# Performance work log

Hardware: AMD Instinct MI355X
Metric: run time of the kernel (lower is better)

Reference implementation:

```python
import jax, jax.numpy as jnp
import numpy as np

DIM, N_HEAD, N_KV, HEAD_DIM = 2048, 16, 4, 128
ROPE_BASE = 10000.0
ROPE_FACTOR = 1.0  # YaRN with factor=1 == plain RoPE


def setup_inputs() -> dict:
    key = jax.random.key(0)
    k1, k2, k3, k4 = jax.random.split(key, 4)
    b, s = 4, 2048
    sc = 1.0 / np.sqrt(DIM)
    return {
        "x": jax.random.normal(k1, (b, s, DIM), dtype=jnp.float32),
        "Wq": jax.random.normal(k2, (DIM, DIM), dtype=jnp.float32) * sc,
        "Wkv": jax.random.normal(k3, (2 * N_KV * HEAD_DIM, DIM), dtype=jnp.float32) * sc,
        "Wo": jax.random.normal(k4, (DIM, DIM), dtype=jnp.float32) * sc,
    }


def _rope_cos_sin(seqlen, start_pos=0):
    inv_freq = 1.0 / (ROPE_BASE ** (jnp.arange(0, HEAD_DIM, 2, dtype=jnp.float32) / HEAD_DIM))
    pos = (jnp.arange(seqlen, dtype=jnp.float32) + start_pos) / ROPE_FACTOR
    ang = pos[:, None] * inv_freq  # (s, hd/2)
    cos = jnp.concatenate([jnp.cos(ang), jnp.cos(ang)], axis=-1)  # (s, hd)
    sin = jnp.concatenate([jnp.sin(ang), jnp.sin(ang)], axis=-1)
    return cos[None, :, None, :], sin[None, :, None, :]  # (1, s, 1, hd)


def _rotate_half(t):
    h = HEAD_DIM // 2
    return jnp.concatenate([-t[..., h:], t[..., :h]], axis=-1)


def reference(x, Wq, Wkv, Wo):
    b, s, dim = x.shape
    G = N_HEAD // N_KV  # query heads per kv head
    q = (x @ Wq.T).reshape(b, s, N_HEAD, HEAD_DIM)                 # (b,s,H,hd)
    kv = (x @ Wkv.T).reshape(b, s, 2, N_KV, HEAD_DIM)
    k, v = kv[:, :, 0], kv[:, :, 1]                                # (b,s,KV,hd)
    cos, sin = _rope_cos_sin(s)
    q = q * cos + _rotate_half(q) * sin
    k = k * cos + _rotate_half(k) * sin
    # grouped attention: head h attends kv head h // G (matches repeat_interleave)
    qg = q.transpose(0, 2, 1, 3).reshape(b, N_KV, G, s, HEAD_DIM)  # (b,KV,G,s,hd)
    kt = k.transpose(0, 2, 1, 3)                                   # (b,KV,s,hd)
    vt = v.transpose(0, 2, 1, 3)
    scale = 1.0 / jnp.sqrt(jnp.asarray(HEAD_DIM, dtype=x.dtype))
    scores = jnp.einsum('bkgqd,bkpd->bkgqp', qg, kt) * scale       # (b,KV,G,s,s)
    causal = jnp.tril(jnp.ones((s, s), dtype=bool))
    scores = jnp.where(causal, scores, jnp.asarray(-jnp.inf, dtype=scores.dtype))
    probs = jax.nn.softmax(scores, axis=-1)
    out = jnp.einsum('bkgqp,bkpd->bkgqd', probs, vt)               # (b,KV,G,s,hd)
    out = out.reshape(b, N_HEAD, s, HEAD_DIM).transpose(0, 2, 1, 3).reshape(b, s, dim)
    return out @ Wo.T
```

## Files before the change

### kernel.cpp

```cpp
#include <hip/hip_runtime.h>
#include <hip/hip_bf16.h>

typedef __hip_bfloat16 bf16;
typedef __attribute__((ext_vector_type(4))) float f32x4;
typedef __attribute__((ext_vector_type(16))) float f32x16;
typedef __attribute__((ext_vector_type(8))) short short8;
typedef __attribute__((ext_vector_type(4))) unsigned u32x4;

#define NHEAD 16
#define NKV 4
#define HD 128
#define BATCH 4
#define SEQ 2048
#define DIMM 2048
#define NROWS (BATCH*SEQ)
#define QKVN (DIMM + 2*NKV*HD)

__device__ inline void gload_lds16(const bf16* g, bf16* l) {
  __builtin_amdgcn_global_load_lds(
      (const __attribute__((address_space(1))) unsigned int*)g,
      (__attribute__((address_space(3))) unsigned int*)l, 16, 0, 0);
}

__device__ inline unsigned cvtpk(float a, float b) {
  unsigned r;
  asm("v_cvt_pk_bf16_f32 %0, %1, %2" : "=v"(r) : "v"(a), "v"(b));
  return r;
}
__device__ inline void pswap(unsigned& x, unsigned& y) {
  asm volatile("v_permlane32_swap_b32 %0, %1" : "+v"(x), "+v"(y));
}
__device__ inline float bf2f(short s) {
  return __uint_as_float(((unsigned)(unsigned short)s) << 16);
}
__device__ inline short f2bfbits(float f) {
  bf16 h = __float2bfloat16(f);
  return *reinterpret_cast<short*>(&h);
}

#define CVTN0 ((size_t)NROWS * DIMM)
#define CVTN1 ((size_t)DIMM * DIMM)
#define CVTN2 ((size_t)2 * NKV * HD * DIMM)
#define CVTN3 ((size_t)DIMM * DIMM)
__global__ void cvt_all(const float* __restrict__ x, const float* __restrict__ wq,
                        const float* __restrict__ wkv, const float* __restrict__ wo,
                        bf16* __restrict__ xb, bf16* __restrict__ wqb,
                        bf16* __restrict__ wkvb, bf16* __restrict__ wob) {
  const size_t total = CVTN0 + CVTN1 + CVTN2 + CVTN3;
  for (size_t i = ((size_t)blockIdx.x * blockDim.x + threadIdx.x) * 4; i < total;
       i += (size_t)gridDim.x * blockDim.x * 4) {
    const float* s;
    bf16* d;
    size_t off;
    if (i < CVTN0) { s = x; d = xb; off = i; }
    else if (i < CVTN0 + CVTN1) { s = wq; d = wqb; off = i - CVTN0; }
    else if (i < CVTN0 + CVTN1 + CVTN2) { s = wkv; d = wkvb; off = i - CVTN0 - CVTN1; }
    else { s = wo; d = wob; off = i - CVTN0 - CVTN1 - CVTN2; }
    const float4 v = *reinterpret_cast<const float4*>(s + off);
    alignas(8) bf16 t[4] = {__float2bfloat16(v.x), __float2bfloat16(v.y),
                            __float2bfloat16(v.z), __float2bfloat16(v.w)};
    *reinterpret_cast<uint2*>(d + off) = *reinterpret_cast<const uint2*>(t);
  }
}

__device__ inline void store_c(float* p, float v) { *p = v; }
__device__ inline void store_c(bf16* p, float v) { *p = __float2bfloat16(v); }

template <typename OutT>
__global__ __launch_bounds__(512, 2) void gemm256(
    const bf16* __restrict__ A, const bf16* __restrict__ B0,
    const bf16* __restrict__ B1, OutT* __restrict__ C,
    int N, int K, int Nsplit, int MI8) {
  __shared__ __align__(16) short As[2][2][256 * 32];
  __shared__ __align__(16) short Bs[2][2][256 * 32];
  const int tid = threadIdx.x;
  const int w = tid >> 6, l = tid & 63;
  const int bid = blockIdx.x;
  const int xcd = bid & 7, q = bid >> 3;
  const int mi = q % MI8, j = q / MI8;
  const int m0 = (xcd * MI8 + mi) * 256, n0 = j * 256;
  const bf16* Ap = A + (size_t)m0 * K;
  const bf16* Bp = (n0 < Nsplit) ? (B0 + (size_t)n0 * K)
                                 : (B1 + (size_t)(n0 - Nsplit) * K);
  const int wr = w >> 2, wc = w & 3;
  const int lr = l & 15, lc = l >> 4;
  const int swz = lc ^ (((lr >> 3) & 1) << 1);

  f32x4 acc[8][4] = {};
  const int KT = K >> 6;

  auto stage = [&](int kt, int kh, int buf) {
#pragma unroll
    for (int jj = 0; jj < 2; ++jj) {
      const int cbase = jj * 512 + w * 64;
      const int ch = cbase + l;
      const int row = ch >> 2, c = ch & 3;
      const int sc = c ^ (((row >> 3) & 1) << 1);
      const int gcol = kt * 64 + kh * 32 + sc * 8;
      gload_lds16(Ap + (size_t)row * K + gcol, (bf16*)&As[buf][kh][cbase * 8]);
      gload_lds16(Bp + (size_t)row * K + gcol, (bf16*)&Bs[buf][kh][cbase * 8]);
    }
  };

  stage(0, 0, 0);
  stage(0, 1, 0);
  stage(1, 0, 1);

  for (int kt = 0; kt < KT; ++kt) {
    const int cur = kt & 1;
#pragma unroll
    for (int kh = 0; kh < 2; ++kh) {
      if (kt < KT - 1) {
        asm volatile("s_waitcnt vmcnt(8)" ::: "memory");
      } else if (kh == 0) {
        asm volatile("s_waitcnt vmcnt(4)" ::: "memory");
      } else {
        asm volatile("s_waitcnt vmcnt(0)" ::: "memory");
      }
      __builtin_amdgcn_s_barrier();
      __builtin_amdgcn_sched_barrier(0);

      short8 a[8], b[4];
      const short* Ab = &As[cur][kh][0];
      const short* Bb = &Bs[cur][kh][0];
#pragma unroll
      for (int mr = 0; mr < 8; ++mr)
        a[mr] = *(const short8*)&Ab[(wr * 128 + mr * 16 + lr) * 32 + swz * 8];
#pragma unroll
      for (int nr = 0; nr < 4; ++nr)
        b[nr] = *(const short8*)&Bb[(wc * 64 + nr * 16 + lr) * 32 + swz * 8];

      {
        const int g = 2 * kt + kh + 3;
        const int st = g >> 1;
        if (st < KT) stage(st, g & 1, st & 1);
      }

      __builtin_amdgcn_s_setprio(1);
#pragma unroll
      for (int mr = 0; mr < 8; ++mr)
#pragma unroll
        for (int nr = 0; nr < 4; ++nr)
          acc[mr][nr] = __builtin_amdgcn_mfma_f32_16x16x32_bf16(
              a[mr], b[nr], acc[mr][nr], 0, 0, 0);
      __builtin_amdgcn_s_setprio(0);
    }
  }

  const int cr4 = (l >> 4) * 4;
#pragma unroll
  for (int mr = 0; mr < 8; ++mr)
#pragma unroll
    for (int nr = 0; nr < 4; ++nr)
#pragma unroll
      for (int r = 0; r < 4; ++r) {
        const int row = m0 + wr * 128 + mr * 16 + cr4 + r;
        const int col = n0 + wc * 64 + nr * 16 + lr;
        store_c(&C[(size_t)row * N + col], acc[mr][nr][r]);
      }
}

#define NVT ((SEQ / 64) * 2 * 16)
#define NRP ((NROWS * 20 * 8) / 256)
__global__ __launch_bounds__(256) void prep_kernel(bf16* __restrict__ qkv,
                                                   bf16* __restrict__ vtg) {
  if ((int)blockIdx.x < NVT) {
    __shared__ short T[64 * 72];
    const int bz = blockIdx.x >> 6;
    const int rem = blockIdx.x & 63;
    const int si = (rem >> 1) * 64;
    const int di = (rem & 1) * 64;
    const int b = bz >> 2, kvh = bz & 3;
    const int t = threadIdx.x;
    const int r = t >> 2, c2 = (t & 3) * 2;
    const bf16* src =
        qkv + (size_t)(b * SEQ + si + r) * QKVN + DIMM + NKV * HD + kvh * 128 + di;
#pragma unroll
    for (int i = 0; i < 2; ++i)
      *(short8*)&T[r * 72 + (c2 + i) * 8] = *(const short8*)(src + (c2 + i) * 8);
    __syncthreads();
#pragma unroll
    for (int i = 0; i < 2; ++i) {
      short8 v;
      const int s8 = (c2 + i) * 8;
#pragma unroll
      for (int j = 0; j < 8; ++j) v[j] = T[(s8 + j) * 72 + r];
      *(short8*)(vtg + (size_t)(kvh * 128 + di + r) * NROWS + b * SEQ + si + s8) = v;
    }
  } else {
    const int idx = ((int)blockIdx.x - NVT) * blockDim.x + threadIdx.x;
    const int dc = idx & 7;
    const int slot = (idx >> 3) % 20;
    const int row = idx / (8 * 20);
    const int col = (slot < 16) ? slot * 128 : DIMM + (slot - 16) * 128;
    const size_t base = (size_t)row * QKVN + col;
    const int pos = row & (SEQ - 1);
    const float psc = (slot < 16) ? 0.12751879895f : 1.0f;
    short8 lo = *(const short8*)(qkv + base + dc * 8);
    short8 hi = *(const short8*)(qkv + base + 64 + dc * 8);
    short8 olo, ohi;
#pragma unroll
    for (int j = 0; j < 8; ++j) {
      const int d = dc * 8 + j;
      const float inv = exp2f((float)d * (-2.0f / 128.0f) * 13.287712379549449f);
      float sn, cs;
      __sincosf((float)pos * inv, &sn, &cs);
      const float flo = bf2f(lo[j]), fhi = bf2f(hi[j]);
      olo[j] = f2bfbits((flo * cs - fhi * sn) * psc);
      ohi[j] = f2bfbits((fhi * cs + flo * sn) * psc);
    }
    *(short8*)(qkv + base + dc * 8) = olo;
    *(short8*)(qkv + base + 64 + dc * 8) = ohi;
  }
}

__global__ __launch_bounds__(512, 2) void attn_kernel(
    const bf16* __restrict__ qkv, const bf16* __restrict__ vtg,
    bf16* __restrict__ aout) {
  __shared__ __align__(16) short KsL[2][64 * 128];
  __shared__ __align__(16) short VtL[2][128 * 64];
  const int tid = threadIdx.x, w = tid >> 6, l = tid & 63;
  const int lq = l & 31, hi = l >> 5;
  const int id = blockIdx.x;
  const int half = id >> 8, rr = id & 255;
  const int bh = (rr >> 3) + half * 32;
  const int j = rr & 7;
  const int qb = half ? j : 7 - j;
  const int b = bh >> 4, h = bh & 15, kvh = h >> 2;
  const int qw0 = qb * 256 + w * 32;
  const int qg = qw0 + lq;

  short8 qf[8];
  {
    const bf16* qptr = qkv + (size_t)(b * SEQ + qg) * QKVN + h * 128 + hi * 8;
#pragma unroll
    for (int s = 0; s < 8; ++s) qf[s] = *(const short8*)(qptr + s * 16);
  }

  f32x16 o[4] = {};
  float m = -1e30f, lsum = 0.f;
  const int ntiles = qb * 4 + 4;

  const bf16* Kgb = qkv + (size_t)(b * SEQ) * QKVN + DIMM + kvh * 128;
  const bf16* Vgb = vtg + (size_t)kvh * 128 * NROWS + b * SEQ;

  auto stage = [&](int kt, int buf) {
#pragma unroll
    for (int rd = 0; rd < 2; ++rd) {
      const int cb = (w * 2 + rd) * 64;
      {
        const int lc = cb + l, k = lc >> 4, c = lc & 15;
        gload_lds16(Kgb + (size_t)(kt * 64 + k) * QKVN + ((c ^ (k & 7)) * 8),
                    (bf16*)&KsL[buf][cb * 8]);
      }
      {
        const int lc = cb + l, d = lc >> 3, c = lc & 7;
        gload_lds16(Vgb + (size_t)d * NROWS + kt * 64 + ((c ^ (d & 7)) * 8),
                    (bf16*)&VtL[buf][cb * 8]);
      }
    }
  };

  stage(0, 0);
  asm volatile("s_waitcnt vmcnt(0)" ::: "memory");
  __builtin_amdgcn_s_barrier();
  __builtin_amdgcn_sched_barrier(0);

  for (int kt = 0; kt < ntiles; ++kt) {
    const int cur = kt & 1;
    if (kt + 1 < ntiles) stage(kt + 1, cur ^ 1);

    if (kt * 64 <= qw0 + 31) {
      f32x16 st[2];
#pragma unroll
      for (int ks = 0; ks < 2; ++ks) {
        const short* kb = &KsL[cur][(ks * 32 + lq) * 128];
        const int r7 = lq & 7;
        f32x16 acc = {};
        __builtin_amdgcn_s_setprio(1);
#pragma unroll
        for (int s = 0; s < 8; ++s) {
          const short8 kf = *(const short8*)&kb[((2 * s + hi) ^ r7) * 8];
          acc = __builtin_amdgcn_mfma_f32_32x32x16_bf16(kf, qf[s], acc, 0, 0, 0);
        }
        __builtin_amdgcn_s_setprio(0);
        st[ks] = acc;
      }
      if (kt * 64 + 63 > qw0) {
#pragma unroll
        for (int ks = 0; ks < 2; ++ks)
#pragma unroll
          for (int r = 0; r < 16; ++r) {
            const int kg = kt * 64 + ks * 32 + (r & 3) + 8 * (r >> 2) + 4 * hi;
            if (kg > qg) st[ks][r] = -1e30f;
          }
      }
      float t[16];
#pragma unroll
      for (int r = 0; r < 16; ++r) t[r] = fmaxf(st[0][r], st[1][r]);
#pragma unroll
      for (int d2 = 8; d2 > 0; d2 >>= 1)
#pragma unroll
        for (int r = 0; r < 8; ++r)
          if (r < d2) t[r] = fmaxf(t[r], t[r + d2]);
      float pm = fmaxf(t[0], __shfl_xor(t[0], 32));
      if (!__all(pm <= m + 11.0f)) {
        const float mnew = fmaxf(m, pm);
        const float fsc = __builtin_amdgcn_exp2f(m - mnew);
        m = mnew;
        lsum *= fsc;
#pragma unroll
        for (int r = 0; r < 16; ++r) {
          const float fq = __shfl(fsc, (r & 3) + 8 * (r >> 2) + 4 * hi);
#pragma unroll
          for (int db = 0; db < 4; ++db) o[db][r] *= fq;
        }
      }
      short8 pa[4];
#pragma unroll
      for (int ks = 0; ks < 2; ++ks) {
        float p[16];
        float s0 = 0.f, s1 = 0.f, s2 = 0.f, s3 = 0.f;
#pragma unroll
        for (int r = 0; r < 16; r += 4) {
          p[r] = __builtin_amdgcn_exp2f(st[ks][r] - m);         s0 += p[r];
          p[r + 1] = __builtin_amdgcn_exp2f(st[ks][r + 1] - m); s1 += p[r + 1];
          p[r + 2] = __builtin_amdgcn_exp2f(st[ks][r + 2] - m); s2 += p[r + 2];
          p[r + 3] = __builtin_amdgcn_exp2f(st[ks][r + 3] - m); s3 += p[r + 3];
        }
        lsum += (s0 + s1) + (s2 + s3);
#pragma unroll
        for (int hf = 0; hf < 2; ++hf) {
          unsigned x0 = cvtpk(p[hf * 8 + 0], p[hf * 8 + 1]);
          unsigned y0 = cvtpk(p[hf * 8 + 4], p[hf * 8 + 5]);
          unsigned x1 = cvtpk(p[hf * 8 + 2], p[hf * 8 + 3]);
          unsigned y1 = cvtpk(p[hf * 8 + 6], p[hf * 8 + 7]);
          pswap(x0, y0);
          pswap(x1, y1);
          union { u32x4 u; short8 s; } pk;
          pk.u = u32x4{x0, x1, y0, y1};
          pa[ks * 2 + hf] = pk.s;
        }
      }
      __builtin_amdgcn_s_setprio(1);
#pragma unroll
      for (int s = 0; s < 4; ++s) {
        const int cc = ((2 * s + hi) ^ (lq & 7)) * 8;
#pragma unroll
        for (int db = 0; db < 4; ++db) {
          const short8 vb = *(const short8*)&VtL[cur][(db * 32 + lq) * 64 + cc];
          o[db] = __builtin_amdgcn_mfma_f32_32x32x16_bf16(pa[s], vb, o[db], 0, 0, 0);
        }
      }
      __builtin_amdgcn_s_setprio(0);
    }

    asm volatile("s_waitcnt vmcnt(0)" ::: "memory");
    __builtin_amdgcn_s_barrier();
    __builtin_amdgcn_sched_barrier(0);
  }

  const float lf = lsum + __shfl_xor(lsum, 32);
#pragma unroll
  for (int r = 0; r < 16; ++r) {
    const int qr = (r & 3) + 8 * (r >> 2) + 4 * hi;
    const float linv = 1.0f / __shfl(lf, qr);
    bf16* op = aout + (size_t)(b * SEQ + qw0 + qr) * DIMM + h * 128 + lq;
#pragma unroll
    for (int db = 0; db < 4; ++db)
      op[db * 32] = __float2bfloat16(o[db][r] * linv);
  }
}

extern "C" void kernel_launch(void* const* d_in, const int* in_sizes, int n_in,
                              void* d_out, int out_size, void* d_ws, size_t ws_size,
                              hipStream_t stream) {
  const float* x = (const float*)d_in[0];
  const float* Wq = (const float*)d_in[1];
  const float* Wkv = (const float*)d_in[2];
  const float* Wo = (const float*)d_in[3];
  float* out = (float*)d_out;

  bf16* xb = (bf16*)d_ws;
  bf16* Wqb = xb + (size_t)NROWS * DIMM;
  bf16* Wkvb = Wqb + (size_t)DIMM * DIMM;
  bf16* Wob = Wkvb + (size_t)2 * NKV * HD * DIMM;
  bf16* attn = Wob + (size_t)DIMM * DIMM;
  bf16* qkv = (bf16*)d_out;
  bf16* vtg = (bf16*)d_out + (size_t)NROWS * QKVN;

  cvt_all<<<2048, 256, 0, stream>>>(x, Wq, Wkv, Wo, xb, Wqb, Wkvb, Wob);

  gemm256<bf16><<<dim3((NROWS / 256) * (QKVN / 256)), 512, 0, stream>>>(
      xb, Wqb, Wkvb, qkv, QKVN, DIMM, DIMM, (NROWS / 256) / 8);

  prep_kernel<<<NVT + NRP, 256, 0, stream>>>(qkv, vtg);

  attn_kernel<<<dim3(512), 512, 0, stream>>>(qkv, vtg, attn);

  gemm256<float><<<dim3((NROWS / 256) * (DIMM / 256)), 512, 0, stream>>>(
      attn, Wob, Wob, out, DIMM, DIMM, DIMM, (NROWS / 256) / 8);
}
```

Measured before the change: 307.3 us.

## Shrink GEMM tile to 128x256 with 32-wide K steps and higher occupancy

Replaces the 256x256 GEMM tile with a 128x256 tile, K steps of 32 and a simpler two-buffer pipeline. Fewer accumulators and less LDS allow four blocks per CU instead of two, which should hide latency better and give more blocks across the grid. The cost is lower arithmetic intensity per block, since A is reused over 256 columns but B only over 128 rows. It also adds an extra barrier per K step, needed because the next stage reuses the current buffer.

```diff
diff --git a/kernel.cpp b/kernel.cpp
--- a/kernel.cpp
+++ b/kernel.cpp
@@ -67,18 +67,18 @@
 __device__ inline void store_c(bf16* p, float v) { *p = __float2bfloat16(v); }
 
 template <typename OutT>
-__global__ __launch_bounds__(512, 2) void gemm256(
+__global__ __launch_bounds__(512, 4) void gemm128(
     const bf16* __restrict__ A, const bf16* __restrict__ B0,
     const bf16* __restrict__ B1, OutT* __restrict__ C,
-    int N, int K, int Nsplit, int MI8) {
-  __shared__ __align__(16) short As[2][2][256 * 32];
-  __shared__ __align__(16) short Bs[2][2][256 * 32];
+    int N, int K, int Nsplit) {
+  __shared__ __align__(16) short As[2][128 * 32];
+  __shared__ __align__(16) short Bs[2][256 * 32];
   const int tid = threadIdx.x;
   const int w = tid >> 6, l = tid & 63;
   const int bid = blockIdx.x;
   const int xcd = bid & 7, q = bid >> 3;
-  const int mi = q % MI8, j = q / MI8;
-  const int m0 = (xcd * MI8 + mi) * 256, n0 = j * 256;
+  const int mi = q & 7, j = q >> 3;
+  const int m0 = (xcd * 8 + mi) * 128, n0 = j * 256;
   const bf16* Ap = A + (size_t)m0 * K;
   const bf16* Bp = (n0 < Nsplit) ? (B0 + (size_t)n0 * K)
                                  : (B1 + (size_t)(n0 - Nsplit) * K);
@@ -86,75 +86,72 @@
   const int lr = l & 15, lc = l >> 4;
   const int swz = lc ^ (((lr >> 3) & 1) << 1);
 
-  f32x4 acc[8][4] = {};
-  const int KT = K >> 6;
-
-  auto stage = [&](int kt, int kh, int buf) {
-#pragma unroll
-    for (int jj = 0; jj < 2; ++jj) {
-      const int cbase = jj * 512 + w * 64;
-      const int ch = cbase + l;
+  f32x4 acc[4][4] = {};
+  const int KT = K >> 5;
+
+  auto stage = [&](int kt, int buf) {
+    {
+      const int cb = w * 64;
+      const int ch = cb + l;
       const int row = ch >> 2, c = ch & 3;
       const int sc = c ^ (((row >> 3) & 1) << 1);
-      const int gcol = kt * 64 + kh * 32 + sc * 8;
-      gload_lds16(Ap + (size_t)row * K + gcol, (bf16*)&As[buf][kh][cbase * 8]);
-      gload_lds16(Bp + (size_t)row * K + gcol, (bf16*)&Bs[buf][kh][cbase * 8]);
+      gload_lds16(Ap + (size_t)row * K + kt * 32 + sc * 8, (bf16*)&As[buf][cb * 8]);
+    }
+#pragma unroll
+    for (int jj = 0; jj < 2; ++jj) {
+      const int cb = jj * 512 + w * 64;
+      const int ch = cb + l;
+      const int row = ch >> 2, c = ch & 3;
+      const int sc = c ^ (((row >> 3) & 1) << 1);
+      gload_lds16(Bp + (size_t)row * K + kt * 32 + sc * 8, (bf16*)&Bs[buf][cb * 8]);
     }
   };
 
-  stage(0, 0, 0);
-  stage(0, 1, 0);
-  stage(1, 0, 1);
+  stage(0, 0);
+  stage(1, 1);
 
   for (int kt = 0; kt < KT; ++kt) {
     const int cur = kt & 1;
-#pragma unroll
-    for (int kh = 0; kh < 2; ++kh) {
-      if (kt < KT - 1) {
-        asm volatile("s_waitcnt vmcnt(8)" ::: "memory");
-      } else if (kh == 0) {
-        asm volatile("s_waitcnt vmcnt(4)" ::: "memory");
-      } else {
-        asm volatile("s_waitcnt vmcnt(0)" ::: "memory");
-      }
-      __builtin_amdgcn_s_barrier();
-      __builtin_amdgcn_sched_barrier(0);
-
-      short8 a[8], b[4];
-      const short* Ab = &As[cur][kh][0];
-      const short* Bb = &Bs[cur][kh][0];
-#pragma unroll
-      for (int mr = 0; mr < 8; ++mr)
-        a[mr] = *(const short8*)&Ab[(wr * 128 + mr * 16 + lr) * 32 + swz * 8];
+    if (kt < KT - 1) {
+      asm volatile("s_waitcnt vmcnt(3)" ::: "memory");
+    } else {
+      asm volatile("s_waitcnt vmcnt(0)" ::: "memory");
+    }
+    __builtin_amdgcn_s_barrier();
+    __builtin_amdgcn_sched_barrier(0);
+
+    short8 a[4], b[4];
+#pragma unroll
+    for (int mr = 0; mr < 4; ++mr)
+      a[mr] = *(const short8*)&As[cur][(wr * 64 + mr * 16 + lr) * 32 + swz * 8];
+#pragma unroll
+    for (int nr = 0; nr < 4; ++nr)
+      b[nr] = *(const short8*)&Bs[cur][(wc * 64 + nr * 16 + lr) * 32 + swz * 8];
+
+    asm volatile("s_waitcnt lgkmcnt(0)" ::: "memory");
+    __builtin_amdgcn_sched_barrier(0);
+    __builtin_amdgcn_s_barrier();
+
+    if (kt + 2 < KT) stage(kt + 2, cur);
+
+    __builtin_amdgcn_s_setprio(1);
+#pragma unroll
+    for (int mr = 0; mr < 4; ++mr)
 #pragma unroll
       for (int nr = 0; nr < 4; ++nr)
-        b[nr] = *(const short8*)&Bb[(wc * 64 + nr * 16 + lr) * 32 + swz * 8];
-
-      {
-        const int g = 2 * kt + kh + 3;
-        const int st = g >> 1;
-        if (st < KT) stage(st, g & 1, st & 1);
-      }
-
-      __builtin_amdgcn_s_setprio(1);
-#pragma unroll
-      for (int mr = 0; mr < 8; ++mr)
-#pragma unroll
-        for (int nr = 0; nr < 4; ++nr)
-          acc[mr][nr] = __builtin_amdgcn_mfma_f32_16x16x32_bf16(
-              a[mr], b[nr], acc[mr][nr], 0, 0, 0);
-      __builtin_amdgcn_s_setprio(0);
-    }
+        acc[mr][nr] = __builtin_amdgcn_mfma_f32_16x16x32_bf16(
+            a[mr], b[nr], acc[mr][nr], 0, 0, 0);
+    __builtin_amdgcn_s_setprio(0);
   }
 
   const int cr4 = (l >> 4) * 4;
 #pragma unroll
-  for (int mr = 0; mr < 8; ++mr)
+  for (int mr = 0; mr < 4; ++mr)
 #pragma unroll
     for (int nr = 0; nr < 4; ++nr)
 #pragma unroll
       for (int r = 0; r < 4; ++r) {
-        const int row = m0 + wr * 128 + mr * 16 + cr4 + r;
+        const int row = m0 + wr * 64 + mr * 16 + cr4 + r;
         const int col = n0 + wc * 64 + nr * 16 + lr;
         store_c(&C[(size_t)row * N + col], acc[mr][nr][r]);
       }
@@ -391,13 +388,13 @@
 
   cvt_all<<<2048, 256, 0, stream>>>(x, Wq, Wkv, Wo, xb, Wqb, Wkvb, Wob);
 
-  gemm256<bf16><<<dim3((NROWS / 256) * (QKVN / 256)), 512, 0, stream>>>(
-      xb, Wqb, Wkvb, qkv, QKVN, DIMM, DIMM, (NROWS / 256) / 8);
+  gemm128<bf16><<<dim3((NROWS / 128) * (QKVN / 256)), 512, 0, stream>>>(
+      xb, Wqb, Wkvb, qkv, QKVN, DIMM, DIMM);
 
   prep_kernel<<<NVT + NRP, 256, 0, stream>>>(qkv, vtg);
 
   attn_kernel<<<dim3(512), 512, 0, stream>>>(qkv, vtg, attn);
 
-  gemm256<float><<<dim3((NROWS / 256) * (DIMM / 256)), 512, 0, stream>>>(
-      attn, Wob, Wob, out, DIMM, DIMM, DIMM, (NROWS / 256) / 8);
-}
+  gemm128<float><<<dim3((NROWS / 128) * (DIMM / 256)), 512, 0, stream>>>(
+      attn, Wob, Wob, out, DIMM, DIMM, DIMM);
+}
```

Measured after the change: 315.1 us. +2.6%, slower.

## Restructure GEMM main loop into 8-phase ping-pong schedule with split A/B staging

Applied to the files above, without the earlier changes.

Replaces the GEMM mainloop's two half-K stages per tile with an eight-phase schedule. Each phase reads a quarter of the A/B fragments from LDS, issues part of the next tile's global-to-LDS loads separately for A and B, and runs a 4x2 subtile of MFMAs between barriers. The goal is to interleave LDS reads, global loads and MFMA work more finely and lower register pressure for fragments. The cost is many more workgroup barriers per K step and lgkmcnt(0) waits that may serialize LDS and MFMA work. It also assumes KT is even.

```diff
diff --git a/kernel.cpp b/kernel.cpp
--- a/kernel.cpp
+++ b/kernel.cpp
@@ -15,6 +15,10 @@
 #define DIMM 2048
 #define NROWS (BATCH*SEQ)
 #define QKVN (DIMM + 2*NKV*HD)
+
+#define SBAR0 __builtin_amdgcn_sched_barrier(0)
+#define BAR   __builtin_amdgcn_s_barrier()
+#define LGKM0 asm volatile("s_waitcnt lgkmcnt(0)" ::: "memory")
 
 __device__ inline void gload_lds16(const bf16* g, bf16* l) {
   __builtin_amdgcn_global_load_lds(
@@ -88,63 +92,94 @@
 
   f32x4 acc[8][4] = {};
   const int KT = K >> 6;
-
-  auto stage = [&](int kt, int kh, int buf) {
+  const int NT2 = KT >> 1;
+
+  auto stageA = [&](int t, int kk) {
+    if (t >= KT) return;
 #pragma unroll
     for (int jj = 0; jj < 2; ++jj) {
-      const int cbase = jj * 512 + w * 64;
-      const int ch = cbase + l;
-      const int row = ch >> 2, c = ch & 3;
+      const int cb = jj * 512 + w * 64;
+      const int G = cb + l;
+      const int row = G >> 2, c = G & 3;
       const int sc = c ^ (((row >> 3) & 1) << 1);
-      const int gcol = kt * 64 + kh * 32 + sc * 8;
-      gload_lds16(Ap + (size_t)row * K + gcol, (bf16*)&As[buf][kh][cbase * 8]);
-      gload_lds16(Bp + (size_t)row * K + gcol, (bf16*)&Bs[buf][kh][cbase * 8]);
-    }
-  };
-
-  stage(0, 0, 0);
-  stage(0, 1, 0);
-  stage(1, 0, 1);
-
-  for (int kt = 0; kt < KT; ++kt) {
-    const int cur = kt & 1;
-#pragma unroll
-    for (int kh = 0; kh < 2; ++kh) {
-      if (kt < KT - 1) {
-        asm volatile("s_waitcnt vmcnt(8)" ::: "memory");
-      } else if (kh == 0) {
-        asm volatile("s_waitcnt vmcnt(4)" ::: "memory");
-      } else {
-        asm volatile("s_waitcnt vmcnt(0)" ::: "memory");
-      }
-      __builtin_amdgcn_s_barrier();
-      __builtin_amdgcn_sched_barrier(0);
-
-      short8 a[8], b[4];
-      const short* Ab = &As[cur][kh][0];
-      const short* Bb = &Bs[cur][kh][0];
-#pragma unroll
-      for (int mr = 0; mr < 8; ++mr)
-        a[mr] = *(const short8*)&Ab[(wr * 128 + mr * 16 + lr) * 32 + swz * 8];
-#pragma unroll
-      for (int nr = 0; nr < 4; ++nr)
-        b[nr] = *(const short8*)&Bb[(wc * 64 + nr * 16 + lr) * 32 + swz * 8];
-
-      {
-        const int g = 2 * kt + kh + 3;
-        const int st = g >> 1;
-        if (st < KT) stage(st, g & 1, st & 1);
-      }
-
-      __builtin_amdgcn_s_setprio(1);
-#pragma unroll
-      for (int mr = 0; mr < 8; ++mr)
-#pragma unroll
-        for (int nr = 0; nr < 4; ++nr)
-          acc[mr][nr] = __builtin_amdgcn_mfma_f32_16x16x32_bf16(
-              a[mr], b[nr], acc[mr][nr], 0, 0, 0);
-      __builtin_amdgcn_s_setprio(0);
-    }
+      gload_lds16(Ap + (size_t)row * K + t * 64 + kk * 32 + sc * 8,
+                  (bf16*)&As[t & 1][kk][cb * 8]);
+    }
+  };
+  auto stageB = [&](int t, int kk) {
+    if (t >= KT) return;
+#pragma unroll
+    for (int jj = 0; jj < 2; ++jj) {
+      const int cb = jj * 512 + w * 64;
+      const int G = cb + l;
+      const int row = G >> 2, c = G & 3;
+      const int sc = c ^ (((row >> 3) & 1) << 1);
+      gload_lds16(Bp + (size_t)row * K + t * 64 + kk * 32 + sc * 8,
+                  (bf16*)&Bs[t & 1][kk][cb * 8]);
+    }
+  };
+
+  short8 afr[8];
+  short8 bfr[8];
+  auto readA = [&](int buf, int msub) {
+#pragma unroll
+    for (int z = 0; z < 8; ++z) {
+      const int mr = z >> 1, kk = z & 1;
+      afr[z] = *(const short8*)&As[buf][kk]
+          [(wr * 128 + msub * 64 + mr * 16 + lr) * 32 + swz * 8];
+    }
+  };
+  auto readB = [&](int buf, int nsub) {
+#pragma unroll
+    for (int z = 0; z < 4; ++z) {
+      const int nr = z >> 1, kk = z & 1;
+      bfr[nsub * 4 + z] = *(const short8*)&Bs[buf][kk]
+          [(wc * 64 + nsub * 32 + nr * 16 + lr) * 32 + swz * 8];
+    }
+  };
+  auto mmac = [&](int msub, int nsub) {
+    __builtin_amdgcn_s_setprio(1);
+#pragma unroll
+    for (int kk = 0; kk < 2; ++kk)
+#pragma unroll
+      for (int mr = 0; mr < 4; ++mr)
+#pragma unroll
+        for (int nr = 0; nr < 2; ++nr)
+          acc[msub * 4 + mr][nsub * 2 + nr] =
+              __builtin_amdgcn_mfma_f32_16x16x32_bf16(
+                  afr[mr * 2 + kk], bfr[nsub * 4 + nr * 2 + kk],
+                  acc[msub * 4 + mr][nsub * 2 + nr], 0, 0, 0);
+    __builtin_amdgcn_s_setprio(0);
+  };
+
+  stageA(0, 0); stageA(0, 1); stageB(0, 0); stageB(0, 1);
+  stageB(1, 0); stageB(1, 1);
+  asm volatile("s_waitcnt vmcnt(4)" ::: "memory");
+  BAR; SBAR0;
+
+  for (int T = 0; T < NT2; ++T) {
+    const int t0 = 2 * T, t1 = 2 * T + 1;
+    const bool last = (T == NT2 - 1);
+    readA(0, 0); readB(0, 0); stageA(t1, 0);
+    SBAR0; BAR; LGKM0; SBAR0; mmac(0, 0); BAR;
+    readB(0, 1); stageA(t1, 1);
+    SBAR0; BAR; LGKM0; SBAR0; mmac(0, 1); BAR;
+    readA(0, 1); stageB(t0 + 2, 0);
+    SBAR0; BAR; LGKM0; SBAR0; mmac(1, 0); BAR;
+    stageB(t0 + 2, 1);
+    if (last) { asm volatile("s_waitcnt vmcnt(0)" ::: "memory"); }
+    else      { asm volatile("s_waitcnt vmcnt(4)" ::: "memory"); }
+    SBAR0; BAR; LGKM0; SBAR0; mmac(1, 1); BAR;
+    readA(1, 0); readB(1, 0); stageA(t0 + 2, 0);
+    SBAR0; BAR; LGKM0; SBAR0; mmac(0, 0); BAR;
+    readB(1, 1); stageA(t0 + 2, 1);
+    SBAR0; BAR; LGKM0; SBAR0; mmac(0, 1); BAR;
+    readA(1, 1); stageB(t1 + 2, 0);
+    SBAR0; BAR; LGKM0; SBAR0; mmac(1, 0); BAR;
+    stageB(t1 + 2, 1);
+    if (last) { asm volatile("s_waitcnt vmcnt(0)" ::: "memory"); }
+    else      { asm volatile("s_waitcnt vmcnt(4)" ::: "memory"); }
+    SBAR0; BAR; LGKM0; SBAR0; mmac(1, 1); BAR;
   }
 
   const int cr4 = (l >> 4) * 4;
```

Measured after the change: 325.5 us. 1.06x slower.
